# Kernel tuning notes

Hardware: AMD Instinct MI355X
Metric: run time of the kernel (lower is better)

The kernel has to match this reference:

```python
import jax, jax.numpy as jnp
import numpy as np

DEPTH = 6
HEADS = 4
DH = 64
MAXLEN = 512

def layer_norm(x, s, b, eps=1e-5):
    m = jnp.mean(x, axis=-1, keepdims=True)
    v = jnp.var(x, axis=-1, keepdims=True)
    return (x - m) / jnp.sqrt(v + eps) * s + b

def setup_inputs() -> dict:
    key = jax.random.key(0)
    ks = jax.random.split(key, 8)
    D = 256
    inner = HEADS * DH  # 256
    hid = 1024          # int(256 * 4.0)
    init = lambda k, shape: jax.random.normal(k, shape, jnp.float32) * 0.02
    return {
        "x": jax.random.normal(ks[0], (8, 12, 512, 256), jnp.float32),
        "ln1_s": jnp.ones((DEPTH, D), jnp.float32), "ln1_b": jnp.zeros((DEPTH, D), jnp.float32),
        "qkv_w": init(ks[1], (DEPTH, D, 3 * inner)), "qkv_b": jnp.zeros((DEPTH, 3 * inner), jnp.float32),
        "proj_w": init(ks[2], (DEPTH, inner, D)), "proj_b": jnp.zeros((DEPTH, D), jnp.float32),
        "rel_table": init(ks[3], (DEPTH, 2 * MAXLEN - 1, HEADS)),
        "ln2_s": jnp.ones((DEPTH, D), jnp.float32), "ln2_b": jnp.zeros((DEPTH, D), jnp.float32),
        "w1": init(ks[4], (DEPTH, D, hid)), "b1": jnp.zeros((DEPTH, hid), jnp.float32),
        "w2": init(ks[5], (DEPTH, hid, D)), "b2": jnp.zeros((DEPTH, D), jnp.float32),
        "lnf_s": jnp.ones((D,), jnp.float32), "lnf_b": jnp.zeros((D,), jnp.float32),
    }

def reference(x, ln1_s, ln1_b, qkv_w, qkv_b, proj_w, proj_b, rel_table,
              ln2_s, ln2_b, w1, b1, w2, b2, lnf_s, lnf_b):
    B, L, N, D = x.shape
    h = x.reshape(B * L, N, D)  # (b l) n d
    idx = jnp.arange(N)
    rel_idx = idx[:, None] - idx[None, :] + MAXLEN - 1  # (N, N) in [0, 2*MAXLEN-2]
    scale = DH ** -0.5
    for d in range(DEPTH):
        # pre-norm attention with relative position bias
        xn = layer_norm(h, ln1_s[d], ln1_b[d])
        qkv = xn @ qkv_w[d] + qkv_b[d]
        q, k, v = jnp.split(qkv, 3, axis=-1)
        split_heads = lambda t: t.reshape(B * L, N, HEADS, DH).transpose(0, 2, 1, 3)
        q, k, v = split_heads(q), split_heads(k), split_heads(v)
        bias = rel_table[d][rel_idx].transpose(2, 0, 1)  # (H, N, N)
        scores = jnp.einsum('bhid,bhjd->bhij', q, k) * scale + bias[None]
        attn = jax.nn.softmax(scores, axis=-1)
        o = jnp.einsum('bhij,bhjd->bhid', attn, v)
        o = o.transpose(0, 2, 1, 3).reshape(B * L, N, HEADS * DH)
        h = h + (o @ proj_w[d] + proj_b[d])
        # pre-norm FFN
        xn2 = layer_norm(h, ln2_s[d], ln2_b[d])
        h = h + (jax.nn.gelu(xn2 @ w1[d] + b1[d]) @ w2[d] + b2[d])
    h = layer_norm(h, lnf_s, lnf_b)
    return h.reshape(B, L, N, D)
```

## Files before the change

### kernel.cpp

```cpp
#include <hip/hip_runtime.h>
#include <math.h>

#define T_TOK 49152
#define DMODEL 256
#define NSEQ 512
#define BLROWS 96
#define LOG2E 1.4426950408889634f

typedef unsigned short ushortT;
using frag_ab = __attribute__((ext_vector_type(8))) short;
using f32x4   = __attribute__((ext_vector_type(4))) float;

__device__ __forceinline__ ushortT f2b(float f) {
    union { float f; unsigned int u; } v; v.f = f;
    unsigned int u = v.u;
    u += 0x7FFFu + ((u >> 16) & 1u);
    return (ushortT)(u >> 16);
}
__device__ __forceinline__ float b2f(ushortT h) {
    union { unsigned int u; float f; } v; v.u = ((unsigned int)h) << 16;
    return v.f;
}

#if __has_builtin(__builtin_amdgcn_exp2f)
#define FEXP2(x) __builtin_amdgcn_exp2f(x)
#else
#define FEXP2(x) __expf((x) * 0.6931471805599453f)
#endif

__device__ __forceinline__ unsigned int cvtpk_bf16(float lo, float hi) {
    unsigned int r;
    asm("v_cvt_pk_bf16_f32 %0, %1, %2" : "=v"(r) : "v"(lo), "v"(hi));
    return r;
}

__device__ __forceinline__ void gload_lds16(const ushortT* g, ushortT* l) {
    __builtin_amdgcn_global_load_lds(
        (const __attribute__((address_space(1))) unsigned int*)g,
        (__attribute__((address_space(3))) unsigned int*)l, 16, 0, 0);
}

__global__ __launch_bounds__(256) void wprep_kernel(const float* __restrict__ qkv_w,
                                                    const float* __restrict__ proj_w,
                                                    const float* __restrict__ w1,
                                                    const float* __restrict__ w2,
                                                    ushortT* __restrict__ out) {
    __shared__ float Ls[64][132];
    int bid = blockIdx.x;
    int d = bid / 96, t = bid % 96;
    const float* src; int N, KS; size_t dbase; int tt;
    if (t < 24)      { src = qkv_w  + (size_t)d * 256 * 768;  N = 768;  KS = 4;  dbase = (size_t)d * 196608;            tt = t;      }
    else if (t < 32) { src = proj_w + (size_t)d * 256 * 256;  N = 256;  KS = 4;  dbase = 1179648 + (size_t)d * 65536;   tt = t - 24; }
    else if (t < 64) { src = w1     + (size_t)d * 256 * 1024; N = 1024; KS = 4;  dbase = 1572864 + (size_t)d * 262144;  tt = t - 32; }
    else             { src = w2     + (size_t)d * 1024 * 256; N = 256;  KS = 16; dbase = 3145728 + (size_t)d * 262144;  tt = t - 64; }
    int nb = tt / KS, ks = tt % KS;
    int k0 = ks * 64, n0 = nb * 128;
    int tid = threadIdx.x;
#pragma unroll
    for (int i = 0; i < 8; ++i) {
        int fidx = tid + i * 256;
        int kk = fidx >> 5, ng = fidx & 31;
        float4 v = *(const float4*)(src + (size_t)(k0 + kk) * N + n0 + ng * 4);
        *(float4*)&Ls[kk][ng * 4] = v;
    }
    __syncthreads();
    int n = tid & 127, kh = tid >> 7;
    ushortT* dst = out + dbase + (size_t)tt * 8192 + n * 64 + kh * 32;
    ushortT tmp[32];
#pragma unroll
    for (int j = 0; j < 32; ++j) tmp[j] = f2b(Ls[kh * 32 + j][n]);
#pragma unroll
    for (int u = 0; u < 4; ++u) *(uint4*)(dst + u * 8) = *(uint4*)(tmp + u * 8);
}

template <bool OB>
__global__ __launch_bounds__(256) void ln_kernel(const float* __restrict__ in,
                                                 void* __restrict__ out,
                                                 const float* __restrict__ s,
                                                 const float* __restrict__ b) {
    int wave = threadIdx.x >> 6;
    int lane = threadIdx.x & 63;
    size_t row = (size_t)blockIdx.x * 4 + wave;
    float4 v = reinterpret_cast<const float4*>(in + row * DMODEL)[lane];
    float sum = v.x + v.y + v.z + v.w;
    float ssq = v.x * v.x + v.y * v.y + v.z * v.z + v.w * v.w;
#pragma unroll
    for (int m = 1; m <= 32; m <<= 1) {
        sum += __shfl_xor(sum, m, 64);
        ssq += __shfl_xor(ssq, m, 64);
    }
    float mean = sum * (1.0f / 256.0f);
    float var = ssq * (1.0f / 256.0f) - mean * mean;
    float rstd = rsqrtf(var + 1e-5f);
    float4 sv = reinterpret_cast<const float4*>(s)[lane];
    float4 bv = reinterpret_cast<const float4*>(b)[lane];
    float o0 = (v.x - mean) * rstd * sv.x + bv.x;
    float o1 = (v.y - mean) * rstd * sv.y + bv.y;
    float o2 = (v.z - mean) * rstd * sv.z + bv.z;
    float o3 = (v.w - mean) * rstd * sv.w + bv.w;
    if (OB) {
        ushortT* po = (ushortT*)out + row * DMODEL + lane * 4;
        ushort4 ov; ov.x = f2b(o0); ov.y = f2b(o1); ov.z = f2b(o2); ov.w = f2b(o3);
        *(ushort4*)po = ov;
    } else {
        float4 ov; ov.x = o0; ov.y = o1; ov.z = o2; ov.w = o3;
        reinterpret_cast<float4*>((float*)out + row * DMODEL)[lane] = ov;
    }
}

template <int EPI>
__global__ __launch_bounds__(256) void gemm_bf16(const ushortT* __restrict__ A,
                                                 const ushortT* __restrict__ Wt,
                                                 const float* __restrict__ bias,
                                                 float* __restrict__ R,
                                                 ushortT* __restrict__ Cb,
                                                 int K, int N) {
    __shared__ ushortT smem[32768];
    const int nb = blockIdx.x, n0 = nb * 128;
    const int m0 = blockIdx.y * 128;
    const int tid = threadIdx.x, lane = tid & 63, wave = tid >> 6;
    const int wr = wave >> 1, wc = wave & 1;
    const int KS = K >> 6;
    const size_t wtile = (size_t)nb * KS * 8192;

    const int rA = lane >> 3;
    const int colsw = (lane & 7) ^ rA;

    auto STAGE = [&](int buf, int kt) {
        ushortT* Ad = smem + buf * 16384;
        ushortT* Bd = Ad + 8192;
#pragma unroll
        for (int c2 = 0; c2 < 4; ++c2) {
            int rb = wave * 32 + c2 * 8;
            int row = rb + rA;
            gload_lds16(A + (size_t)(m0 + row) * K + kt * 64 + colsw * 8,
                        Ad + rb * 64);
            gload_lds16(Wt + wtile + (size_t)kt * 8192 + row * 64 + colsw * 8,
                        Bd + rb * 64);
        }
    };

    f32x4 acc[4][4];
#pragma unroll
    for (int i = 0; i < 4; ++i)
#pragma unroll
        for (int j = 0; j < 4; ++j) acc[i][j] = (f32x4)0.0f;

    STAGE(0, 0);
    __syncthreads();
    int cur = 0;
    for (int kt = 0; kt < KS; ++kt) {
        if (kt + 1 < KS) STAGE(cur ^ 1, kt + 1);
        const ushortT* Ab = smem + cur * 16384;
        const ushortT* Bb = Ab + 8192;
#pragma unroll
        for (int kst = 0; kst < 2; ++kst) {
            frag_ab af[4], bf4[4];
            int ku = kst * 4 + (lane >> 4);
#pragma unroll
            for (int f = 0; f < 4; ++f) {
                int row = wr * 64 + f * 16 + (lane & 15);
                af[f] = *(const frag_ab*)&Ab[row * 64 + ((ku ^ (row & 7)) << 3)];
                int col = wc * 64 + f * 16 + (lane & 15);
                bf4[f] = *(const frag_ab*)&Bb[col * 64 + ((ku ^ (col & 7)) << 3)];
            }
#pragma unroll
            for (int mf = 0; mf < 4; ++mf)
#pragma unroll
                for (int nf = 0; nf < 4; ++nf)
                    acc[mf][nf] = __builtin_amdgcn_mfma_f32_16x16x32_bf16(
                        af[mf], bf4[nf], acc[mf][nf], 0, 0, 0);
        }
        __syncthreads();
        cur ^= 1;
    }

    const int cg = lane >> 4, cl = lane & 15;
    if (EPI != 2) {
        ushortT* Cs = smem;
#pragma unroll
        for (int nf = 0; nf < 4; ++nf) {
            int col = wc * 64 + nf * 16 + cl;
            float bv = bias[n0 + col];
#pragma unroll
            for (int mf = 0; mf < 4; ++mf)
#pragma unroll
                for (int r = 0; r < 4; ++r) {
                    int row = wr * 64 + mf * 16 + cg * 4 + r;
                    float c = acc[mf][nf][r] + bv;
                    if (EPI == 1) {
                        c = c / (1.0f + __expf(-1.5957691216f * (c + 0.044715f * c * c * c)));
                    }
                    Cs[row * 128 + (((col >> 3) ^ (row & 7)) << 3) + (col & 7)] = f2b(c);
                }
        }
        __syncthreads();
#pragma unroll
        for (int it = 0; it < 8; ++it) {
            int idx = tid + it * 256;
            int row = idx >> 4, u = idx & 15;
            uint4 v = *(uint4*)&Cs[row * 128 + ((u ^ (row & 7)) << 3)];
            *(uint4*)&Cb[(size_t)(m0 + row) * N + n0 + u * 8] = v;
        }
    } else {
        float* Cf = (float*)smem;
#pragma unroll
        for (int h = 0; h < 2; ++h) {
            if (wr == h) {
#pragma unroll
                for (int nf = 0; nf < 4; ++nf) {
                    int col = wc * 64 + nf * 16 + cl;
                    float bv = bias[n0 + col];
#pragma unroll
                    for (int mf = 0; mf < 4; ++mf)
#pragma unroll
                        for (int r = 0; r < 4; ++r) {
                            int rl = mf * 16 + cg * 4 + r;
                            Cf[rl * 128 + (((col >> 2) ^ (rl & 7)) << 2) + (col & 3)] =
                                acc[mf][nf][r] + bv;
                        }
                }
            }
            __syncthreads();
#pragma unroll
            for (int it = 0; it < 8; ++it) {
                int idx = tid + it * 256;
                int row2 = idx >> 5, u = idx & 31;
                float4 c4 = *(float4*)&Cf[row2 * 128 + ((u ^ (row2 & 7)) << 2)];
                float* rp = R + (size_t)(m0 + h * 64 + row2) * N + n0 + u * 4;
                float4 r4 = *(float4*)rp;
                r4.x += c4.x; r4.y += c4.y; r4.z += c4.z; r4.w += c4.w;
                *(float4*)rp = r4;
            }
            if (h == 0) __syncthreads();
        }
    }
}

__global__ __launch_bounds__(512) void attn_kernel(const ushortT* __restrict__ qkv,
                                                   const float* __restrict__ rel,
                                                   ushortT* __restrict__ o) {
    __shared__ ushortT Ks[64 * 64];
    __shared__ ushortT Vt[64 * 72];
    __shared__ ushortT Ps[128 * 64];
    __shared__ float   rl[1024];

    const int pair = blockIdx.x, qb = blockIdx.y;
    const int bl = pair >> 2, hh = pair & 3;
    const int tid = threadIdx.x;
    const int lane = tid & 63, w = tid >> 6;
    const int c15 = lane & 15, g = lane >> 4;
    const size_t base = (size_t)bl * NSEQ * 768;
    const int qoff = hh * 64, koff = 256 + hh * 64, voff = 512 + hh * 64;
    const int i0 = qb * 128;

    for (int i = tid; i < 1023; i += 512) rl[i] = rel[(size_t)i * 4 + hh] * LOG2E;

    frag_ab qf[2];
    {
        const ushortT* qp = qkv + base + (size_t)(i0 + w * 16 + c15) * 768 + qoff + g * 8;
        qf[0] = *(const frag_ab*)(qp);
        qf[1] = *(const frag_ab*)(qp + 32);
    }

    float m_i[4], l_i[4];
    f32x4 oacc[4];
#pragma unroll
    for (int r = 0; r < 4; ++r) { m_i[r] = -1e30f; l_i[r] = 0.0f; }
#pragma unroll
    for (int nf = 0; nf < 4; ++nf) oacc[nf] = (f32x4)0.0f;

    const int irow = w * 16 + g * 4;

    for (int kt = 0; kt < 8; ++kt) {
        __syncthreads();
        {
            int j = tid >> 3, dg = tid & 7;
            const ushortT* kp = qkv + base + (size_t)(kt * 64 + j) * 768;
            uint4 kv4 = *(const uint4*)(kp + koff + dg * 8);
            *(uint4*)&Ks[j * 64 + ((dg ^ (j & 7)) << 3)] = kv4;
            uint4 vv4 = *(const uint4*)(kp + voff + dg * 8);
            ushortT tmp[8];
            *(uint4*)tmp = vv4;
            int jc = j ^ (dg << 3);
#pragma unroll
            for (int e = 0; e < 8; ++e) Vt[(dg * 8 + e) * 72 + jc] = tmp[e];
        }
        __syncthreads();

        f32x4 sacc[4];
#pragma unroll
        for (int nf = 0; nf < 4; ++nf) sacc[nf] = (f32x4)0.0f;
#pragma unroll
        for (int kst = 0; kst < 2; ++kst) {
            int ku = kst * 4 + g;
#pragma unroll
            for (int nf = 0; nf < 4; ++nf) {
                int j = nf * 16 + c15;
                frag_ab kf = *(frag_ab*)&Ks[j * 64 + ((ku ^ (j & 7)) << 3)];
                sacc[nf] = __builtin_amdgcn_mfma_f32_16x16x32_bf16(qf[kst], kf, sacc[nf], 0, 0, 0);
            }
        }

        float sv[4][4];
        const int rlb = i0 + irow - kt * 64 - c15 + 511;
#pragma unroll
        for (int nf = 0; nf < 4; ++nf)
#pragma unroll
            for (int r = 0; r < 4; ++r)
                sv[nf][r] = sacc[nf][r] * (0.125f * LOG2E) + rl[rlb + r - nf * 16];

        float rmax[4];
#pragma unroll
        for (int r = 0; r < 4; ++r) {
            float rm = fmaxf(fmaxf(sv[0][r], sv[1][r]), fmaxf(sv[2][r], sv[3][r]));
#pragma unroll
            for (int m = 1; m <= 8; m <<= 1) rm = fmaxf(rm, __shfl_xor(rm, m, 64));
            rmax[r] = rm;
        }
        bool cskip = true;
#pragma unroll
        for (int r = 0; r < 4; ++r) cskip = cskip && (rmax[r] <= m_i[r] + 11.5f);
        if (!__all(cskip)) {
#pragma unroll
            for (int r = 0; r < 4; ++r) {
                float mn = fmaxf(m_i[r], rmax[r]);
                float cr = FEXP2(m_i[r] - mn);
                m_i[r] = mn;
                l_i[r] *= cr;
#pragma unroll
                for (int nf = 0; nf < 4; ++nf) oacc[nf][r] *= cr;
            }
        }

        float psum[4] = {0.0f, 0.0f, 0.0f, 0.0f};
        unsigned int words[4][4];
#pragma unroll
        for (int nf = 0; nf < 4; ++nf)
#pragma unroll
            for (int r = 0; r < 4; ++r) {
                float p = FEXP2(sv[nf][r] - m_i[r]);
                psum[r] += p;
                float po = __shfl_xor(p, 1, 64);
                words[nf][r] = cvtpk_bf16(p, po);
            }
#pragma unroll
        for (int r = 0; r < 4; ++r) {
#pragma unroll
            for (int m = 1; m <= 8; m <<= 1) psum[r] += __shfl_xor(psum[r], m, 64);
            l_i[r] += psum[r];
        }

        if (!(lane & 1)) {
#pragma unroll
            for (int nf = 0; nf < 4; ++nf) {
                int j2 = nf * 16 + c15;
#pragma unroll
                for (int r = 0; r < 4; ++r) {
                    int i = irow + r;
                    *(unsigned int*)&Ps[i * 64 + ((((j2 >> 3) ^ (i & 7))) << 3) + (j2 & 7)] =
                        words[nf][r];
                }
            }
        }

#pragma unroll
        for (int ks2 = 0; ks2 < 2; ++ks2) {
            int ip = w * 16 + c15;
            int jb = ks2 * 32 + g * 8;
            frag_ab pf = *(frag_ab*)&Ps[ip * 64 + (((jb >> 3) ^ (ip & 7)) << 3)];
#pragma unroll
            for (int nf = 0; nf < 4; ++nf) {
                int dh = nf * 16 + c15;
                int jv = jb ^ ((dh >> 3) << 3);
                frag_ab vf = *(frag_ab*)&Vt[dh * 72 + jv];
                oacc[nf] = __builtin_amdgcn_mfma_f32_16x16x32_bf16(pf, vf, oacc[nf], 0, 0, 0);
            }
        }
    }

    float inv[4];
#pragma unroll
    for (int r = 0; r < 4; ++r) inv[r] = 1.0f / l_i[r];
#pragma unroll
    for (int nf = 0; nf < 4; ++nf)
#pragma unroll
        for (int r = 0; r < 4; ++r) {
            float own = oacc[nf][r] * inv[r];
            float other = __shfl_xor(own, 1, 64);
            if (!(lane & 1)) {
                size_t trow = (size_t)bl * NSEQ + i0 + irow + r;
                *(unsigned int*)&o[trow * DMODEL + hh * 64 + nf * 16 + c15] =
                    cvtpk_bf16(own, other);
            }
        }
}

extern "C" void kernel_launch(void* const* d_in, const int* in_sizes, int n_in,
                              void* d_out, int out_size, void* d_ws, size_t ws_size,
                              hipStream_t stream) {
    const float* x       = (const float*)d_in[0];
    const float* ln1_s   = (const float*)d_in[1];
    const float* ln1_b   = (const float*)d_in[2];
    const float* qkv_w   = (const float*)d_in[3];
    const float* qkv_b   = (const float*)d_in[4];
    const float* proj_w  = (const float*)d_in[5];
    const float* proj_b  = (const float*)d_in[6];
    const float* rel_tab = (const float*)d_in[7];
    const float* ln2_s   = (const float*)d_in[8];
    const float* ln2_b   = (const float*)d_in[9];
    const float* w1      = (const float*)d_in[10];
    const float* b1      = (const float*)d_in[11];
    const float* w2      = (const float*)d_in[12];
    const float* b2      = (const float*)d_in[13];
    const float* lnf_s   = (const float*)d_in[14];
    const float* lnf_b   = (const float*)d_in[15];

    float* h = (float*)d_out;
    ushortT* wsu = (ushortT*)d_ws;
    const size_t WPRE = 4718592;

    static const int cands[12] = {1, 2, 3, 4, 6, 8, 12, 16, 24, 32, 48, 96};
    int NC = 96;
    for (int i = 0; i < 12; ++i) {
        size_t tc = (size_t)T_TOK / cands[i];
        if (WPRE * 2 + tc * 3072 <= ws_size) { NC = cands[i]; break; }
    }
    const int TC = T_TOK / NC;
    const int BLC = BLROWS / NC;
    ushortT* xnC = wsu + WPRE;
    ushortT* big = xnC + (size_t)TC * 256;
    ushortT* oC  = big + (size_t)TC * 1024;

    wprep_kernel<<<576, 256, 0, stream>>>(qkv_w, proj_w, w1, w2, wsu);
    hipMemcpyAsync(h, x, (size_t)T_TOK * DMODEL * sizeof(float),
                   hipMemcpyDeviceToDevice, stream);

    dim3 blk(256);
    for (int d = 0; d < 6; ++d) {
        for (int c = 0; c < NC; ++c) {
            float* hc = h + (size_t)c * TC * DMODEL;
            ln_kernel<true><<<TC / 4, blk, 0, stream>>>(hc, xnC, ln1_s + d * 256, ln1_b + d * 256);
            gemm_bf16<0><<<dim3(6, TC / 128), blk, 0, stream>>>(
                xnC, wsu + (size_t)d * 196608, qkv_b + d * 768, nullptr, big, 256, 768);
            attn_kernel<<<dim3(BLC * 4, NSEQ / 128), 512, 0, stream>>>(
                big, rel_tab + (size_t)d * 1023 * 4, oC);
            gemm_bf16<2><<<dim3(2, TC / 128), blk, 0, stream>>>(
                oC, wsu + 1179648 + (size_t)d * 65536, proj_b + d * 256, hc, nullptr, 256, 256);
        }
        for (int c = 0; c < NC; ++c) {
            float* hc = h + (size_t)c * TC * DMODEL;
            ln_kernel<true><<<TC / 4, blk, 0, stream>>>(hc, xnC, ln2_s + d * 256, ln2_b + d * 256);
            gemm_bf16<1><<<dim3(8, TC / 128), blk, 0, stream>>>(
                xnC, wsu + 1572864 + (size_t)d * 262144, b1 + d * 1024, nullptr, big, 256, 1024);
            gemm_bf16<2><<<dim3(2, TC / 128), blk, 0, stream>>>(
                big, wsu + 3145728 + (size_t)d * 262144, b2 + d * 256, hc, nullptr, 1024, 256);
        }
    }
    ln_kernel<false><<<T_TOK / 4, blk, 0, stream>>>(h, h, lnf_s, lnf_b);
}
```

Baseline: 2.051 ms.

## Double-buffer K/V tiles in attention with async LDS loads and MFMA priority

```diff
diff --git a/kernel.cpp b/kernel.cpp
--- a/kernel.cpp
+++ b/kernel.cpp
@@ -240,8 +240,8 @@
 __global__ __launch_bounds__(512) void attn_kernel(const ushortT* __restrict__ qkv,
                                                    const float* __restrict__ rel,
                                                    ushortT* __restrict__ o) {
-    __shared__ ushortT Ks[64 * 64];
-    __shared__ ushortT Vt[64 * 72];
+    __shared__ ushortT Ks[2][64 * 64];
+    __shared__ ushortT Vt[2][64 * 72];
     __shared__ ushortT Ps[128 * 64];
     __shared__ float   rl[1024];
 
@@ -256,9 +256,27 @@
 
     for (int i = tid; i < 1023; i += 512) rl[i] = rel[(size_t)i * 4 + hh] * LOG2E;
 
+    const int sj = tid >> 3, sdg = tid & 7;
+    const ushortT* kvb = qkv + base;
+    auto KSTAGE = [&](int buf, int kt) {
+        gload_lds16(kvb + (size_t)(kt * 64 + sj) * 768 + koff + ((sdg ^ (sj & 7)) << 3),
+                    &Ks[buf][0] + (size_t)w * 512);
+    };
+    uint4 vreg;
+    auto VLOAD = [&](int kt) {
+        vreg = *(const uint4*)(kvb + (size_t)(kt * 64 + sj) * 768 + voff + sdg * 8);
+    };
+    auto VWRITE = [&](int buf) {
+        ushortT tmp[8];
+        *(uint4*)tmp = vreg;
+        int jc = sj ^ (sdg << 3);
+#pragma unroll
+        for (int e = 0; e < 8; ++e) Vt[buf][(sdg * 8 + e) * 72 + jc] = tmp[e];
+    };
+
     frag_ab qf[2];
     {
-        const ushortT* qp = qkv + base + (size_t)(i0 + w * 16 + c15) * 768 + qoff + g * 8;
+        const ushortT* qp = kvb + (size_t)(i0 + w * 16 + c15) * 768 + qoff + g * 8;
         qf[0] = *(const frag_ab*)(qp);
         qf[1] = *(const frag_ab*)(qp + 32);
     }
@@ -272,35 +290,30 @@
 
     const int irow = w * 16 + g * 4;
 
+    VLOAD(0);
+    KSTAGE(0, 0);
+    VWRITE(0);
+    __syncthreads();
+
+    int cur = 0;
     for (int kt = 0; kt < 8; ++kt) {
-        __syncthreads();
-        {
-            int j = tid >> 3, dg = tid & 7;
-            const ushortT* kp = qkv + base + (size_t)(kt * 64 + j) * 768;
-            uint4 kv4 = *(const uint4*)(kp + koff + dg * 8);
-            *(uint4*)&Ks[j * 64 + ((dg ^ (j & 7)) << 3)] = kv4;
-            uint4 vv4 = *(const uint4*)(kp + voff + dg * 8);
-            ushortT tmp[8];
-            *(uint4*)tmp = vv4;
-            int jc = j ^ (dg << 3);
-#pragma unroll
-            for (int e = 0; e < 8; ++e) Vt[(dg * 8 + e) * 72 + jc] = tmp[e];
-        }
-        __syncthreads();
+        if (kt < 7) { KSTAGE(cur ^ 1, kt + 1); VLOAD(kt + 1); }
 
         f32x4 sacc[4];
 #pragma unroll
         for (int nf = 0; nf < 4; ++nf) sacc[nf] = (f32x4)0.0f;
+        __builtin_amdgcn_s_setprio(1);
 #pragma unroll
         for (int kst = 0; kst < 2; ++kst) {
             int ku = kst * 4 + g;
 #pragma unroll
             for (int nf = 0; nf < 4; ++nf) {
                 int j = nf * 16 + c15;
-                frag_ab kf = *(frag_ab*)&Ks[j * 64 + ((ku ^ (j & 7)) << 3)];
+                frag_ab kf = *(frag_ab*)&Ks[cur][j * 64 + ((ku ^ (j & 7)) << 3)];
                 sacc[nf] = __builtin_amdgcn_mfma_f32_16x16x32_bf16(qf[kst], kf, sacc[nf], 0, 0, 0);
             }
         }
+        __builtin_amdgcn_s_setprio(0);
 
         float sv[4][4];
         const int rlb = i0 + irow - kt * 64 - c15 + 511;
@@ -351,6 +364,8 @@
             l_i[r] += psum[r];
         }
 
+        if (kt < 7) VWRITE(cur ^ 1);
+
         if (!(lane & 1)) {
 #pragma unroll
             for (int nf = 0; nf < 4; ++nf) {
@@ -364,6 +379,7 @@
             }
         }
 
+        __builtin_amdgcn_s_setprio(1);
 #pragma unroll
         for (int ks2 = 0; ks2 < 2; ++ks2) {
             int ip = w * 16 + c15;
@@ -373,10 +389,14 @@
             for (int nf = 0; nf < 4; ++nf) {
                 int dh = nf * 16 + c15;
                 int jv = jb ^ ((dh >> 3) << 3);
-                frag_ab vf = *(frag_ab*)&Vt[dh * 72 + jv];
+                frag_ab vf = *(frag_ab*)&Vt[cur][dh * 72 + jv];
                 oacc[nf] = __builtin_amdgcn_mfma_f32_16x16x32_bf16(pf, vf, oacc[nf], 0, 0, 0);
             }
         }
+        __builtin_amdgcn_s_setprio(0);
+
+        __syncthreads();
+        cur ^= 1;
     }
 
     float inv[4];
```

Result: no change. 2.081 ms (+1.5%).
